# Kernel optimization log

Measured on AMD Instinct MI355X. Metric: run time of the kernel, lower is better.

## Reference

```python
import jax, jax.numpy as jnp
import numpy as np

MAX_DISP = 4  # max_displacement
PAD = MAX_DISP
ODIM = 2 * MAX_DISP + 1  # 9 -> 81 cost-volume channels


def setup_inputs() -> dict:
    key = jax.random.key(0)
    k1, k2 = jax.random.split(key)
    B, C, H, W = 4, 256, 96, 192
    x1 = jax.random.normal(k1, (B, C, H, W), dtype=jnp.float32)
    x2 = jax.random.normal(k2, (B, C, H, W), dtype=jnp.float32)
    return {"x1": x1, "x2": x2}


def reference(x1, x2):
    B, C, H, W = x1.shape
    # zero-pad x2 spatially by PAD on each side (matches F.pad([pad]*4))
    x2p = jnp.pad(x2, ((0, 0), (0, 0), (PAD, PAD), (PAD, PAD)))
    cv = []
    for i in range(ODIM):          # fixed 9x9 displacement grid
        for j in range(ODIM):
            shifted = jax.lax.dynamic_slice(
                x2p, (0, 0, i, j), (B, C, H, W))
            # mean over channel dim -> [B, H, W]
            cv.append(jnp.mean(x1 * shifted, axis=1))
    return jnp.stack(cv, axis=1)  # [B, 81, H, W]
```

## Files before the change

### kernel.cpp

```cpp
#include <hip/hip_runtime.h>
#include <stddef.h>


#define NB 4
#define NC 256
#define HH 96
#define WW 192
#define TW 16
#define TH 8
#define KC 32
#define NROWS 16
#define CHW (HH * WW)
#define KSTRIDE (KC * CHW)

#define KS 264
#define RS 1096
#define XBI(row, kg, n) ((row) * RS + (kg) * KS + (n) * 8)

typedef __attribute__((ext_vector_type(8))) short bf16x8;
typedef __attribute__((ext_vector_type(4))) float f32x4;

__device__ __forceinline__ unsigned short f2bf(float f) {
    union { float f; unsigned u; } c; c.f = f;
    unsigned r = c.u + 0x7FFFu + ((c.u >> 16) & 1u);
    return (unsigned short)(r >> 16);
}

__global__ __launch_bounds__(512, 4) void corr_mfma(
    const float* __restrict__ x1, const float* __restrict__ x2,
    float* __restrict__ out)
{
    __shared__ union {
        unsigned short xb[NROWS * RS];
        float band[TH][9][9][18];
    } lds;

    const int lin = blockIdx.x;
    const int sw  = (lin & 7) * 72 + (lin >> 3);
    const int b   = sw / 144;
    const int t2  = sw - b * 144;
    const int ty  = t2 / 12;
    const int tx  = t2 - ty * 12;

    const int tid  = threadIdx.x;
    const int wv   = tid >> 6;
    const int lane = tid & 63;
    const int col  = lane & 15;
    const int q    = lane >> 4;
    const int w0   = tx * TW;
    const int h0   = ty * TH;
    const int h    = h0 + wv;

    f32x4 acc[9][2];
#pragma unroll
    for (int di = 0; di < 9; ++di) {
        acc[di][0] = (f32x4)0.0f;
        acc[di][1] = (f32x4)0.0f;
    }

    unsigned o2k[3];
    int      lofk[3];
    bool     okk[3];
#pragma unroll
    for (int k = 0; k < 3; ++k) {
        const int t   = tid + k * 512;
        const int seg = t % 6;
        const int u   = t / 6;
        const int cp  = u & 15;
        const int row = u >> 4;
        const int gh  = h0 - 4 + row;
        const int gw  = w0 - 4 + seg * 4;
        okk[k] = (gh >= 0) & (gh < HH) & (gw >= 0) & (gw <= WW - 4);
        const int ghc = gh < 0 ? 0 : (gh > HH - 1 ? HH - 1 : gh);
        const int gwc = gw < 0 ? 0 : gw;
        o2k[k]  = (unsigned)(((b * NC + cp * 2) * HH + ghc) * WW + gwc);
        lofk[k] = XBI(row, cp >> 2, seg * 4) + (cp & 3) * 2;
    }
    unsigned o1 = (unsigned)(((b * NC + q * 8) * HH + h) * WW + w0 + col);

    float pf[24];
    float pa[8];

#define STAGE_LOAD()                                                     \
    {                                                                    \
        _Pragma("unroll")                                                \
        for (int k = 0; k < 3; ++k) {                                    \
            _Pragma("unroll")                                            \
            for (int e = 0; e < 2; ++e) {                                \
                float4 ld = make_float4(0.f, 0.f, 0.f, 0.f);             \
                if (okk[k]) ld = *(const float4*)&x2[o2k[k] + e * CHW];  \
                *(float4*)&pf[(k * 2 + e) * 4] = ld;                     \
            }                                                            \
            o2k[k] += KSTRIDE;                                           \
        }                                                                \
    }

#define X1_LOAD()                                                        \
    {                                                                    \
        _Pragma("unroll")                                                \
        for (int j = 0; j < 8; ++j) pa[j] = x1[o1 + j * CHW];            \
        o1 += KSTRIDE;                                                   \
    }

    STAGE_LOAD();
    X1_LOAD();

    const int rbase = XBI(wv, q, col);

    for (int ci = 0; ci < 8; ++ci) {
#pragma unroll
        for (int k = 0; k < 3; ++k) {
#pragma unroll
            for (int p = 0; p < 4; ++p) {
                ushort2 v;
                v.x = f2bf(pf[(k * 2 + 0) * 4 + p]);
                v.y = f2bf(pf[(k * 2 + 1) * 4 + p]);
                *(ushort2*)&lds.xb[lofk[k] + p * 8] = v;
            }
        }
        if (ci < 7) STAGE_LOAD();
        __syncthreads();

        bf16x8 a;
#pragma unroll
        for (int j = 0; j < 8; ++j) a[j] = (short)f2bf(pa[j]);
        if (ci < 7) X1_LOAD();

#pragma unroll
        for (int di = 0; di < 9; ++di) {
            bf16x8 b0 = *(const bf16x8*)&lds.xb[rbase + di * RS];
            bf16x8 b1 = *(const bf16x8*)&lds.xb[rbase + di * RS + 128];
            acc[di][0] = __builtin_amdgcn_mfma_f32_16x16x32_bf16(a, b0, acc[di][0], 0, 0, 0);
            acc[di][1] = __builtin_amdgcn_mfma_f32_16x16x32_bf16(a, b1, acc[di][1], 0, 0, 0);
        }
        __syncthreads();
    }

#pragma unroll
    for (int di = 0; di < 9; ++di)
#pragma unroll
        for (int half = 0; half < 2; ++half)
#pragma unroll
            for (int r = 0; r < 4; ++r) {
                int m  = q * 4 + r;
                int dj = half * 16 + col - m;
                if (dj >= 0 && dj < 9)
                    lds.band[wv][di][dj][m] = acc[di][half][r];
            }
    __syncthreads();

    const float scale = 1.0f / 256.0f;
#pragma unroll
    for (int it = 0; it < 21; ++it) {
        int combo = it * 4 + q;
        if (combo < 81) {
            float v = lds.band[wv][combo / 9][combo % 9][col];
            out[((size_t)((b * 81 + combo) * HH + h)) * WW + w0 + col] = v * scale;
        }
    }
}

extern "C" void kernel_launch(void* const* d_in, const int* in_sizes, int n_in,
                              void* d_out, int out_size, void* d_ws, size_t ws_size,
                              hipStream_t stream) {
    const float* x1 = (const float*)d_in[0];
    const float* x2 = (const float*)d_in[1];
    float* out = (float*)d_out;

    dim3 grid(576);
    corr_mfma<<<grid, 512, 0, stream>>>(x1, x2, out);
}
```

Before: 220.9 us.

## Halve tile height and split displacement MFMAs across wave pairs

Tile height drops from 8 to 4 rows, so the grid doubles to 1152 blocks. Each of the 8 waves now covers one output row and half of the 18 displacement MFMAs, which cuts accumulator registers in half. The x2 staging loads move after the barrier so they overlap the MFMA work, and inactive loader threads are masked. The trade-off is more halo reloading per output, since 12 staged rows now serve 4 output rows instead of 16 serving 8, and each wave's x1 fragment is loaded twice.

```diff
diff --git a/kernel.cpp b/kernel.cpp
--- a/kernel.cpp
+++ b/kernel.cpp
@@ -7,11 +7,12 @@
 #define HH 96
 #define WW 192
 #define TW 16
-#define TH 8
+#define TH 4
 #define KC 32
-#define NROWS 16
+#define NROWS 12
 #define CHW (HH * WW)
 #define KSTRIDE (KC * CHW)
+#define NTASK 1152
 
 #define KS 264
 #define RS 1096
@@ -36,9 +37,9 @@
     } lds;
 
     const int lin = blockIdx.x;
-    const int sw  = (lin & 7) * 72 + (lin >> 3);
-    const int b   = sw / 144;
-    const int t2  = sw - b * 144;
+    const int sw  = (lin & 7) * 144 + (lin >> 3);
+    const int b   = sw / 288;
+    const int t2  = sw - b * 288;
     const int ty  = t2 / 12;
     const int tx  = t2 - ty * 12;
 
@@ -47,34 +48,36 @@
     const int lane = tid & 63;
     const int col  = lane & 15;
     const int q    = lane >> 4;
+    const int r    = wv & 3;
+    const int dig  = wv >> 2;
     const int w0   = tx * TW;
     const int h0   = ty * TH;
-    const int h    = h0 + wv;
+    const int h    = h0 + r;
 
-    f32x4 acc[9][2];
+    f32x4 acc[9];
 #pragma unroll
-    for (int di = 0; di < 9; ++di) {
-        acc[di][0] = (f32x4)0.0f;
-        acc[di][1] = (f32x4)0.0f;
-    }
+    for (int s = 0; s < 9; ++s) acc[s] = (f32x4)0.0f;
 
     unsigned o2k[3];
     int      lofk[3];
     bool     okk[3];
+    bool     act[3];
 #pragma unroll
     for (int k = 0; k < 3; ++k) {
         const int t   = tid + k * 512;
+        act[k] = (t < NTASK);
         const int seg = t % 6;
         const int u   = t / 6;
         const int cp  = u & 15;
         const int row = u >> 4;
         const int gh  = h0 - 4 + row;
         const int gw  = w0 - 4 + seg * 4;
-        okk[k] = (gh >= 0) & (gh < HH) & (gw >= 0) & (gw <= WW - 4);
+        okk[k] = act[k] & (gh >= 0) & (gh < HH) & (gw >= 0) & (gw <= WW - 4);
         const int ghc = gh < 0 ? 0 : (gh > HH - 1 ? HH - 1 : gh);
         const int gwc = gw < 0 ? 0 : gw;
+        const int rwc = row > NROWS - 1 ? NROWS - 1 : row;
         o2k[k]  = (unsigned)(((b * NC + cp * 2) * HH + ghc) * WW + gwc);
-        lofk[k] = XBI(row, cp >> 2, seg * 4) + (cp & 3) * 2;
+        lofk[k] = XBI(rwc, cp >> 2, seg * 4) + (cp & 3) * 2;
     }
     unsigned o1 = (unsigned)(((b * NC + q * 8) * HH + h) * WW + w0 + col);
 
@@ -105,57 +108,66 @@
     STAGE_LOAD();
     X1_LOAD();
 
-    const int rbase = XBI(wv, q, col);
+    const int rbase = XBI(r, q, col);
 
     for (int ci = 0; ci < 8; ++ci) {
 #pragma unroll
         for (int k = 0; k < 3; ++k) {
+            if (act[k]) {
 #pragma unroll
-            for (int p = 0; p < 4; ++p) {
-                ushort2 v;
-                v.x = f2bf(pf[(k * 2 + 0) * 4 + p]);
-                v.y = f2bf(pf[(k * 2 + 1) * 4 + p]);
-                *(ushort2*)&lds.xb[lofk[k] + p * 8] = v;
+                for (int p = 0; p < 4; ++p) {
+                    ushort2 v;
+                    v.x = f2bf(pf[(k * 2 + 0) * 4 + p]);
+                    v.y = f2bf(pf[(k * 2 + 1) * 4 + p]);
+                    *(ushort2*)&lds.xb[lofk[k] + p * 8] = v;
+                }
             }
         }
-        if (ci < 7) STAGE_LOAD();
         __syncthreads();
 
         bf16x8 a;
 #pragma unroll
         for (int j = 0; j < 8; ++j) a[j] = (short)f2bf(pa[j]);
-        if (ci < 7) X1_LOAD();
+        if (ci < 7) {
+            STAGE_LOAD();
+            X1_LOAD();
+        }
 
 #pragma unroll
-        for (int di = 0; di < 9; ++di) {
-            bf16x8 b0 = *(const bf16x8*)&lds.xb[rbase + di * RS];
-            bf16x8 b1 = *(const bf16x8*)&lds.xb[rbase + di * RS + 128];
-            acc[di][0] = __builtin_amdgcn_mfma_f32_16x16x32_bf16(a, b0, acc[di][0], 0, 0, 0);
-            acc[di][1] = __builtin_amdgcn_mfma_f32_16x16x32_bf16(a, b1, acc[di][1], 0, 0, 0);
+        for (int s = 0; s < 9; ++s) {
+            const int u    = dig * 9 + s;
+            const int di   = u >> 1;
+            const int half = u & 1;
+            bf16x8 bb = *(const bf16x8*)&lds.xb[rbase + di * RS + half * 128];
+            acc[s] = __builtin_amdgcn_mfma_f32_16x16x32_bf16(a, bb, acc[s], 0, 0, 0);
         }
         __syncthreads();
     }
 
 #pragma unroll
-    for (int di = 0; di < 9; ++di)
+    for (int s = 0; s < 9; ++s) {
+        const int u  = dig * 9 + s;
+        const int di = u >> 1;
+        const int uh = u & 1;
 #pragma unroll
-        for (int half = 0; half < 2; ++half)
-#pragma unroll
-            for (int r = 0; r < 4; ++r) {
-                int m  = q * 4 + r;
-                int dj = half * 16 + col - m;
-                if (dj >= 0 && dj < 9)
-                    lds.band[wv][di][dj][m] = acc[di][half][r];
-            }
+        for (int rg = 0; rg < 4; ++rg) {
+            int m  = q * 4 + rg;
+            int dj = uh * 16 + col - m;
+            if (dj >= 0 && dj < 9)
+                lds.band[r][di][dj][m] = acc[s][rg];
+        }
+    }
     __syncthreads();
 
     const float scale = 1.0f / 256.0f;
 #pragma unroll
-    for (int it = 0; it < 21; ++it) {
-        int combo = it * 4 + q;
-        if (combo < 81) {
-            float v = lds.band[wv][combo / 9][combo % 9][col];
-            out[((size_t)((b * 81 + combo) * HH + h)) * WW + w0 + col] = v * scale;
+    for (int it = 0; it < 11; ++it) {
+        int gi = it * 32 + (tid >> 4);
+        if (gi < 324) {
+            int combo = gi >> 2;
+            int row   = gi & 3;
+            float v = lds.band[row][combo / 9][combo % 9][tid & 15];
+            out[((size_t)((b * 81 + combo) * HH + h0 + row)) * WW + w0 + (tid & 15)] = v * scale;
         }
     }
 }
@@ -167,6 +179,6 @@
     const float* x2 = (const float*)d_in[1];
     float* out = (float*)d_out;
 
-    dim3 grid(576);
+    dim3 grid(1152);
     corr_mfma<<<grid, 512, 0, stream>>>(x1, x2, out);
 }
```

After: 215.2 us. 2.5% less time.
